# Kernel tuning notes

Measured on AMD Instinct MI355X. Metric: run time of the kernel, lower is better.

Reference implementation:

```python
import jax, jax.numpy as jnp
import numpy as np

B, C, E, H = 8, 2048, 1024, 128


def setup_inputs() -> dict:
    key = jax.random.key(0)
    kx, kq, kk, kv = jax.random.split(key, 4)
    scale = 1.0 / np.sqrt(E)
    return {
        "x": jax.random.normal(kx, (B, C, E), dtype=jnp.float32),
        "Wq": jax.random.normal(kq, (E, H), dtype=jnp.float32) * scale,
        "Wk": jax.random.normal(kk, (E, H), dtype=jnp.float32) * scale,
        "Wv": jax.random.normal(kv, (E, H), dtype=jnp.float32) * scale,
    }


def reference(x, Wq, Wk, Wv):
    # x: (B, C, E); projections -> (B, C, H)
    q = jnp.einsum("bce,eh->bch", x, Wq)
    k = jnp.einsum("bce,eh->bch", x, Wk)
    v = jnp.einsum("bce,eh->bch", x, Wv)
    # NOTE: original scales by sqrt(embed_size), not head_size
    scores = jnp.einsum("bqh,bkh->bqk", q, k) / jnp.sqrt(jnp.asarray(E, x.dtype))
    Cq = x.shape[1]
    causal = jnp.tril(jnp.ones((Cq, Cq), dtype=bool))
    scores = jnp.where(causal, scores, -jnp.inf)
    weights = jax.nn.softmax(scores, axis=-1)  # (B, C, C)
    out = jnp.einsum("bqk,bkh->bqh", weights, v)
    return out
```

## Files before the change

### kernel.cpp

```cpp
#include <hip/hip_runtime.h>
#include <hip/hip_bf16.h>

#define BATCH 8
#define CTX   2048
#define EMB   1024
#define HD    128
#define VSTR  2080

using bf16x8 = __attribute__((ext_vector_type(8))) short;
using fx4    = __attribute__((ext_vector_type(4))) float;

__device__ __forceinline__ ushort f2bf(float f) {
    union { float f; unsigned u; } v; v.f = f;
    unsigned u = v.u;
    u += 0x7fffu + ((u >> 16) & 1u);
    return (ushort)(u >> 16);
}

__device__ __forceinline__ unsigned cvtpk(float a, float b) {
    unsigned r;
    asm("v_cvt_pk_bf16_f32 %0, %1, %2" : "=v"(r) : "v"(a), "v"(b));
    return r;
}

__device__ __forceinline__ void gload16(const void* g, void* l) {
    __builtin_amdgcn_global_load_lds(
        (const __attribute__((address_space(1))) unsigned*)g,
        (__attribute__((address_space(3))) unsigned*)l, 16, 0, 0);
}

__global__ void wt_kernel(const float* __restrict__ Wq, const float* __restrict__ Wk,
                          const float* __restrict__ Wv, ushort* __restrict__ Wt) {
    int idx = blockIdx.x * blockDim.x + threadIdx.x;
    int e = idx % EMB;
    int h = (idx / EMB) % HD;
    int w = idx / (EMB * HD);
    const float* W = (w == 0) ? Wq : (w == 1) ? Wk : Wv;
    Wt[idx] = f2bf(W[e * HD + h]);
}

__global__ __launch_bounds__(256) void proj_kernel(
        const float* __restrict__ x, const ushort* __restrict__ Wt,
        ushort* __restrict__ q, ushort* __restrict__ k, ushort* __restrict__ vt) {
    __shared__ __align__(16) char As[3][4096];
    __shared__ __align__(16) char Bs[2][24576];

    const int t    = threadIdx.x;
    const int wave = t >> 6;
    const int lane = t & 63;
    const int lo = lane & 15, hi = lane >> 4;
    const int brow = blockIdx.x * 32;

    fx4 acc[2][6];
#pragma unroll
    for (int m2 = 0; m2 < 2; m2++)
#pragma unroll
        for (int n = 0; n < 6; n++) acc[m2][n] = fx4{0.f, 0.f, 0.f, 0.f};

    const int arow  = t >> 3;
    const int aslot = (t & 7) ^ (arow & 7);
    const float* asrc = x + (size_t)(brow + arow) * EMB + aslot * 4;

    const ushort* bsrc[6];
#pragma unroll
    for (int r = 0; r < 6; r++) {
        const int lrow = r * 32 + (t >> 3);
        const int u    = (t & 7) ^ (lrow & 7);
        bsrc[r] = Wt + (size_t)(lrow * 2 + (u >> 2)) * EMB + (u & 3) * 8;
    }

    gload16(asrc + 0, As[0] + wave * 1024);
#pragma unroll
    for (int r = 0; r < 6; ++r)
        gload16(bsrc[r] + 0, Bs[0] + r * 4096 + wave * 1024);
    gload16(asrc + 32, As[1] + wave * 1024);

    for (int it = 0; it < 32; ++it) {
        if (it == 31) asm volatile("s_waitcnt vmcnt(0)" ::: "memory");
        else          asm volatile("s_waitcnt vmcnt(1)" ::: "memory");
        __builtin_amdgcn_sched_barrier(0);
        __builtin_amdgcn_s_barrier();
        __builtin_amdgcn_sched_barrier(0);

        if (it + 1 < 32) {
#pragma unroll
            for (int r = 0; r < 6; ++r)
                gload16(bsrc[r] + (it + 1) * 32, Bs[(it + 1) & 1] + r * 4096 + wave * 1024);
            if (it + 2 < 32)
                gload16(asrc + (it + 2) * 32, As[(it + 2) % 3] + wave * 1024);
        }

        const char* Ab = As[it % 3];
        const char* Bb = Bs[it & 1];

        bf16x8 af[2];
#pragma unroll
        for (int m2 = 0; m2 < 2; m2++) {
            const int rowA = m2 * 16 + lo;
            const int s0 = (hi * 2) ^ (rowA & 7);
            const int s1 = (hi * 2 + 1) ^ (rowA & 7);
            fx4 a0 = *(const fx4*)(Ab + rowA * 128 + s0 * 16);
            fx4 a1 = *(const fx4*)(Ab + rowA * 128 + s1 * 16);
            union { unsigned u[4]; bf16x8 v; } pk;
            pk.u[0] = cvtpk(a0[0], a0[1]);
            pk.u[1] = cvtpk(a0[2], a0[3]);
            pk.u[2] = cvtpk(a1[0], a1[1]);
            pk.u[3] = cvtpk(a1[2], a1[3]);
            af[m2] = pk.v;
        }
        __builtin_amdgcn_s_setprio(1);
#pragma unroll
        for (int n = 0; n < 6; n++) {
            const int col  = wave * 96 + n * 16 + lo;
            const int rowp = col >> 1;
            const int slot = ((col & 1) * 4 + hi) ^ (rowp & 7);
            bf16x8 bfr = *(const bf16x8*)(Bb + rowp * 128 + slot * 16);
#pragma unroll
            for (int m2 = 0; m2 < 2; m2++)
                acc[m2][n] = __builtin_amdgcn_mfma_f32_16x16x32_bf16(af[m2], bfr, acc[m2][n], 0, 0, 0);
        }
        __builtin_amdgcn_s_setprio(0);
    }

    const float qscale = 0.03125f;
#pragma unroll
    for (int n = 0; n < 6; n++) {
        const int col = wave * 96 + n * 16 + lo;
        const int bnn = col >> 7;
        const int cc  = col & 127;
#pragma unroll
        for (int m2 = 0; m2 < 2; m2++) {
#pragma unroll
            for (int j = 0; j < 4; j++) {
                const int r = brow + m2 * 16 + hi * 4 + j;
                if (bnn == 0)      q[(size_t)r * HD + cc] = f2bf(acc[m2][n][j] * qscale);
                else if (bnn == 1) k[(size_t)r * HD + cc] = f2bf(acc[m2][n][j]);
                else {
                    const int bb = r >> 11, ccc = r & (CTX - 1);
                    vt[((size_t)bb * HD + cc) * VSTR + ccc] = f2bf(acc[m2][n][j]);
                }
            }
        }
    }
}

__global__ __launch_bounds__(256) void attn_kernel(
        const ushort* __restrict__ q, const ushort* __restrict__ k,
        const ushort* __restrict__ vt, float* __restrict__ out) {
    __shared__ __align__(16) char Ks[2][16384];
    __shared__ __align__(16) char Vs[2][16384];
    __shared__ __align__(16) char p_lds[4][1024];

    const int id   = blockIdx.x;
    const int b    = id & 7;
    const int pos  = id >> 3;
    const int qt   = (pos < 32) ? (63 - pos) : (pos - 32);
    const int t    = threadIdx.x;
    const int wave = t >> 6;
    const int lane = t & 63;
    const int lo = lane & 15, hi = lane >> 4;
    const int wq = wave & 1, w = wave >> 1;
    const int q0 = qt * 32 + wq * 16;

    const ushort* qb = q  + (size_t)b * CTX * HD;
    const ushort* kb = k  + (size_t)b * CTX * HD;
    const ushort* vb = vt + (size_t)b * HD * VSTR;

    bf16x8 qf[4];
#pragma unroll
    for (int ks = 0; ks < 4; ks++)
        qf[ks] = *(const bf16x8*)(qb + (q0 + lo) * HD + ks * 32 + hi * 8);

    fx4 o[8];
#pragma unroll
    for (int h = 0; h < 8; h++) o[h] = fx4{0.f, 0.f, 0.f, 0.f};
    float m[4], l[4];
#pragma unroll
    for (int j = 0; j < 4; j++) { m[j] = 0.f; l[j] = 0.f; }

#define STAGE(bi, kv0_) do {                                                   \
    _Pragma("unroll")                                                          \
    for (int r = 0; r < 4; ++r) {                                              \
        const int row = r * 16 + (t >> 4);                                     \
        gload16(kb + (size_t)((kv0_) + row) * HD + (((t & 15) ^ (row & 7)) << 3), \
                Ks[bi] + r * 4096 + wave * 1024);                              \
    }                                                                          \
    _Pragma("unroll")                                                          \
    for (int r = 0; r < 4; ++r) {                                              \
        const int row = r * 32 + (t >> 3);                                     \
        gload16(vb + (size_t)row * VSTR + (kv0_) + (((t & 7) ^ (row & 7)) << 3), \
                Vs[bi] + r * 4096 + wave * 1024);                              \
    }                                                                          \
} while (0)

    const int nkv = qt / 2 + 1;
    STAGE(0, 0);
    for (int it = 0; it < nkv; ++it) {
        asm volatile("s_waitcnt vmcnt(0)" ::: "memory");
        __builtin_amdgcn_sched_barrier(0);
        __builtin_amdgcn_s_barrier();
        __builtin_amdgcn_sched_barrier(0);
        if (it + 1 < nkv) STAGE((it + 1) & 1, (it + 1) * 64);

        const char* Kb = Ks[it & 1];
        const char* Vb = Vs[it & 1];
        const int kv0 = it * 64;

        fx4 s[2];
        s[0] = fx4{0.f, 0.f, 0.f, 0.f};
        s[1] = fx4{0.f, 0.f, 0.f, 0.f};
        __builtin_amdgcn_s_setprio(1);
#pragma unroll
        for (int n2 = 0; n2 < 2; n2++) {
            const int row = w * 32 + n2 * 16 + lo;
            const unsigned sw = (unsigned)((row & 7) << 4);
#pragma unroll
            for (int ks = 0; ks < 4; ks++) {
                bf16x8 kf = *(const bf16x8*)(Kb + row * 256 + ((ks * 64 + hi * 16) ^ sw));
                s[n2] = __builtin_amdgcn_mfma_f32_16x16x32_bf16(qf[ks], kf, s[n2], 0, 0, 0);
            }
        }
        __builtin_amdgcn_s_setprio(0);

        const bool diag = (kv0 + 64 > q0);
        float pmax[4];
        int allok = 1;
#pragma unroll
        for (int j = 0; j < 4; j++) {
            const int r = q0 + hi * 4 + j;
            if (diag) {
#pragma unroll
                for (int n2 = 0; n2 < 2; n2++)
                    if ((kv0 + w * 32 + n2 * 16 + lo) > r) s[n2][j] = -INFINITY;
            }
            pmax[j] = fmaxf(s[0][j], s[1][j]);
            allok &= (pmax[j] <= m[j] + 16.0f);
        }
        if (!__all(allok)) {
#pragma unroll
            for (int j = 0; j < 4; j++) {
                float mx = pmax[j];
                mx = fmaxf(mx, __shfl_xor(mx, 1));
                mx = fmaxf(mx, __shfl_xor(mx, 2));
                mx = fmaxf(mx, __shfl_xor(mx, 4));
                mx = fmaxf(mx, __shfl_xor(mx, 8));
                const float mn = fmaxf(m[j], mx);
                const float f  = __expf(m[j] - mn);
                l[j] *= f;
#pragma unroll
                for (int h = 0; h < 8; h++) o[h][j] *= f;
                m[j] = mn;
            }
        }
#pragma unroll
        for (int j = 0; j < 4; j++) {
            float sum = 0.f;
#pragma unroll
            for (int n2 = 0; n2 < 2; n2++) {
                const float pv = __expf(s[n2][j] - m[j]);
                s[n2][j] = pv;
                sum += pv;
            }
            l[j] += sum;
            const int row = hi * 4 + j;
            const unsigned sw = (unsigned)((row & 3) << 4);
#pragma unroll
            for (int n2 = 0; n2 < 2; n2++) {
                const unsigned cb = (unsigned)((n2 * 16 + lo) * 2);
                *(ushort*)(p_lds[wave] + row * 64 + (cb ^ sw)) = f2bf(s[n2][j]);
            }
        }
        asm volatile("" ::: "memory");
        bf16x8 pa = *(const bf16x8*)(p_lds[wave] + lo * 64 + ((hi * 16) ^ ((lo & 3) << 4)));
        __builtin_amdgcn_s_setprio(1);
#pragma unroll
        for (int h = 0; h < 8; h++) {
            const int vr = h * 16 + lo;
            bf16x8 vf = *(const bf16x8*)(Vb + vr * 128 + ((w * 64 + hi * 16) ^ ((vr & 7) << 4)));
            o[h] = __builtin_amdgcn_mfma_f32_16x16x32_bf16(pa, vf, o[h], 0, 0, 0);
        }
        __builtin_amdgcn_s_setprio(0);
    }
#undef STAGE

#pragma unroll
    for (int j = 0; j < 4; j++) {
        l[j] += __shfl_xor(l[j], 1);
        l[j] += __shfl_xor(l[j], 2);
        l[j] += __shfl_xor(l[j], 4);
        l[j] += __shfl_xor(l[j], 8);
    }

    float* oB  = (float*)Ks[0];
    float* mlB = (float*)Vs[0];
    __syncthreads();
    if (w == 1) {
#pragma unroll
        for (int j = 0; j < 4; j++) {
            const int row = hi * 4 + j;
            if (lo == 0) { mlB[wq * 32 + row] = m[j]; mlB[wq * 32 + 16 + row] = l[j]; }
#pragma unroll
            for (int h = 0; h < 8; h++)
                oB[(wq * 16 + row) * 128 + h * 16 + lo] = o[h][j];
        }
    }
    __syncthreads();
    if (w == 0) {
        float* ob = out + ((size_t)b * CTX + q0) * HD;
#pragma unroll
        for (int j = 0; j < 4; j++) {
            const int row = hi * 4 + j;
            const float mB = mlB[wq * 32 + row], lB = mlB[wq * 32 + 16 + row];
            const float mt = fmaxf(m[j], mB);
            const float fA = __expf(m[j] - mt);
            const float fB = __expf(mB - mt);
            const float inv = 1.0f / (l[j] * fA + lB * fB);
#pragma unroll
            for (int h = 0; h < 8; h++)
                ob[row * HD + h * 16 + lo] =
                    (o[h][j] * fA + oB[(wq * 16 + row) * 128 + h * 16 + lo] * fB) * inv;
        }
    }
}

extern "C" void kernel_launch(void* const* d_in, const int* in_sizes, int n_in,
                              void* d_out, int out_size, void* d_ws, size_t ws_size,
                              hipStream_t stream) {
    const float* x  = (const float*)d_in[0];
    const float* Wq = (const float*)d_in[1];
    const float* Wk = (const float*)d_in[2];
    const float* Wv = (const float*)d_in[3];

    ushort* Wt = (ushort*)d_ws;
    ushort* qw = (ushort*)((char*)d_ws + 786432);
    ushort* kw = qw + (size_t)BATCH * CTX * HD;
    ushort* vw = kw + (size_t)BATCH * CTX * HD;

    wt_kernel<<<(3 * HD * EMB) / 256, 256, 0, stream>>>(Wq, Wk, Wv, Wt);
    proj_kernel<<<(BATCH * CTX) / 32, 256, 0, stream>>>(x, Wt, qw, kw, vw);
    attn_kernel<<<512, 256, 0, stream>>>(qw, kw, vw, (float*)d_out);
}
```

Before: 96.83 us.

## Load projection operands directly from global into registers, split columns across blocks

The projection GEMM stops staging x and weight tiles through LDS with barriers and instead has each lane load its MFMA fragments straight from global memory into double-buffered registers. The grid gains a second dimension that splits the 384 output columns into two halves of 192, so each block computes a 32x192 tile. This removes LDS traffic and block-wide synchronisation and doubles the number of blocks. In exchange, the fp32 x rows are now read twice from global memory and the per-lane loads are less coalesced.

```diff
diff --git a/kernel.cpp b/kernel.cpp
--- a/kernel.cpp
+++ b/kernel.cpp
@@ -42,90 +42,68 @@
 __global__ __launch_bounds__(256) void proj_kernel(
         const float* __restrict__ x, const ushort* __restrict__ Wt,
         ushort* __restrict__ q, ushort* __restrict__ k, ushort* __restrict__ vt) {
-    __shared__ __align__(16) char As[3][4096];
-    __shared__ __align__(16) char Bs[2][24576];
-
     const int t    = threadIdx.x;
     const int wave = t >> 6;
     const int lane = t & 63;
     const int lo = lane & 15, hi = lane >> 4;
     const int brow = blockIdx.x * 32;
-
-    fx4 acc[2][6];
+    const int bcol = blockIdx.y * 192;
+
+    const float*  a0p = x + (size_t)(brow + lo) * EMB + hi * 8;
+    const float*  a1p = a0p + (size_t)16 * EMB;
+    const ushort* b0p = Wt + (size_t)(bcol + wave * 48 + lo) * EMB + hi * 8;
+    const ushort* b1p = b0p + (size_t)16 * EMB;
+    const ushort* b2p = b0p + (size_t)32 * EMB;
+
+    fx4 acc[2][3];
 #pragma unroll
     for (int m2 = 0; m2 < 2; m2++)
 #pragma unroll
-        for (int n = 0; n < 6; n++) acc[m2][n] = fx4{0.f, 0.f, 0.f, 0.f};
-
-    const int arow  = t >> 3;
-    const int aslot = (t & 7) ^ (arow & 7);
-    const float* asrc = x + (size_t)(brow + arow) * EMB + aslot * 4;
-
-    const ushort* bsrc[6];
-#pragma unroll
-    for (int r = 0; r < 6; r++) {
-        const int lrow = r * 32 + (t >> 3);
-        const int u    = (t & 7) ^ (lrow & 7);
-        bsrc[r] = Wt + (size_t)(lrow * 2 + (u >> 2)) * EMB + (u & 3) * 8;
-    }
-
-    gload16(asrc + 0, As[0] + wave * 1024);
-#pragma unroll
-    for (int r = 0; r < 6; ++r)
-        gload16(bsrc[r] + 0, Bs[0] + r * 4096 + wave * 1024);
-    gload16(asrc + 32, As[1] + wave * 1024);
-
+        for (int n = 0; n < 3; n++) acc[m2][n] = fx4{0.f, 0.f, 0.f, 0.f};
+
+    fx4    ab[2][4];
+    bf16x8 bb[2][3];
+
+    ab[0][0] = *(const fx4*)(a0p);     ab[0][1] = *(const fx4*)(a0p + 4);
+    ab[0][2] = *(const fx4*)(a1p);     ab[0][3] = *(const fx4*)(a1p + 4);
+    bb[0][0] = *(const bf16x8*)(b0p);
+    bb[0][1] = *(const bf16x8*)(b1p);
+    bb[0][2] = *(const bf16x8*)(b2p);
+
+#pragma unroll
     for (int it = 0; it < 32; ++it) {
-        if (it == 31) asm volatile("s_waitcnt vmcnt(0)" ::: "memory");
-        else          asm volatile("s_waitcnt vmcnt(1)" ::: "memory");
-        __builtin_amdgcn_sched_barrier(0);
-        __builtin_amdgcn_s_barrier();
-        __builtin_amdgcn_sched_barrier(0);
-
+        const int cur = it & 1, nxt = cur ^ 1;
         if (it + 1 < 32) {
-#pragma unroll
-            for (int r = 0; r < 6; ++r)
-                gload16(bsrc[r] + (it + 1) * 32, Bs[(it + 1) & 1] + r * 4096 + wave * 1024);
-            if (it + 2 < 32)
-                gload16(asrc + (it + 2) * 32, As[(it + 2) % 3] + wave * 1024);
-        }
-
-        const char* Ab = As[it % 3];
-        const char* Bb = Bs[it & 1];
-
+            const int off = (it + 1) * 32;
+            ab[nxt][0] = *(const fx4*)(a0p + off);
+            ab[nxt][1] = *(const fx4*)(a0p + off + 4);
+            ab[nxt][2] = *(const fx4*)(a1p + off);
+            ab[nxt][3] = *(const fx4*)(a1p + off + 4);
+            bb[nxt][0] = *(const bf16x8*)(b0p + off);
+            bb[nxt][1] = *(const bf16x8*)(b1p + off);
+            bb[nxt][2] = *(const bf16x8*)(b2p + off);
+        }
         bf16x8 af[2];
 #pragma unroll
         for (int m2 = 0; m2 < 2; m2++) {
-            const int rowA = m2 * 16 + lo;
-            const int s0 = (hi * 2) ^ (rowA & 7);
-            const int s1 = (hi * 2 + 1) ^ (rowA & 7);
-            fx4 a0 = *(const fx4*)(Ab + rowA * 128 + s0 * 16);
-            fx4 a1 = *(const fx4*)(Ab + rowA * 128 + s1 * 16);
             union { unsigned u[4]; bf16x8 v; } pk;
-            pk.u[0] = cvtpk(a0[0], a0[1]);
-            pk.u[1] = cvtpk(a0[2], a0[3]);
-            pk.u[2] = cvtpk(a1[0], a1[1]);
-            pk.u[3] = cvtpk(a1[2], a1[3]);
+            pk.u[0] = cvtpk(ab[cur][m2 * 2][0], ab[cur][m2 * 2][1]);
+            pk.u[1] = cvtpk(ab[cur][m2 * 2][2], ab[cur][m2 * 2][3]);
+            pk.u[2] = cvtpk(ab[cur][m2 * 2 + 1][0], ab[cur][m2 * 2 + 1][1]);
+            pk.u[3] = cvtpk(ab[cur][m2 * 2 + 1][2], ab[cur][m2 * 2 + 1][3]);
             af[m2] = pk.v;
         }
-        __builtin_amdgcn_s_setprio(1);
-#pragma unroll
-        for (int n = 0; n < 6; n++) {
-            const int col  = wave * 96 + n * 16 + lo;
-            const int rowp = col >> 1;
-            const int slot = ((col & 1) * 4 + hi) ^ (rowp & 7);
-            bf16x8 bfr = *(const bf16x8*)(Bb + rowp * 128 + slot * 16);
+#pragma unroll
+        for (int n = 0; n < 3; n++)
 #pragma unroll
             for (int m2 = 0; m2 < 2; m2++)
-                acc[m2][n] = __builtin_amdgcn_mfma_f32_16x16x32_bf16(af[m2], bfr, acc[m2][n], 0, 0, 0);
-        }
-        __builtin_amdgcn_s_setprio(0);
+                acc[m2][n] = __builtin_amdgcn_mfma_f32_16x16x32_bf16(af[m2], bb[cur][n], acc[m2][n], 0, 0, 0);
     }
 
     const float qscale = 0.03125f;
 #pragma unroll
-    for (int n = 0; n < 6; n++) {
-        const int col = wave * 96 + n * 16 + lo;
+    for (int n = 0; n < 3; n++) {
+        const int col = bcol + wave * 48 + n * 16 + lo;
         const int bnn = col >> 7;
         const int cc  = col & 127;
 #pragma unroll
@@ -136,8 +114,8 @@
                 if (bnn == 0)      q[(size_t)r * HD + cc] = f2bf(acc[m2][n][j] * qscale);
                 else if (bnn == 1) k[(size_t)r * HD + cc] = f2bf(acc[m2][n][j]);
                 else {
-                    const int bb = r >> 11, ccc = r & (CTX - 1);
-                    vt[((size_t)bb * HD + cc) * VSTR + ccc] = f2bf(acc[m2][n][j]);
+                    const int bb2 = r >> 11, ccc = r & (CTX - 1);
+                    vt[((size_t)bb2 * HD + cc) * VSTR + ccc] = f2bf(acc[m2][n][j]);
                 }
             }
         }
@@ -337,6 +315,6 @@
     ushort* vw = kw + (size_t)BATCH * CTX * HD;
 
     wt_kernel<<<(3 * HD * EMB) / 256, 256, 0, stream>>>(Wq, Wk, Wv, Wt);
-    proj_kernel<<<(BATCH * CTX) / 32, 256, 0, stream>>>(x, Wt, qw, kw, vw);
+    proj_kernel<<<dim3(512, 2), 256, 0, stream>>>(x, Wt, qw, kw, vw);
     attn_kernel<<<512, 256, 0, stream>>>(qw, kw, vw, (float*)d_out);
 }
```

After: 160.3 us. 65.6% more time.
